# Kernel optimization log

Measured on AMD Instinct MI355X. Metric: run time of the kernel, lower is better.

Reference implementation:

```python
import jax, jax.numpy as jnp
import numpy as np

OMEGA_ENC = 0.01   # Encoder.omega
OMEGA_K = 0.1      # KernelMLP.omega
N0, E0 = 4096, 16384     # level-0 graph
N1, E1 = 1024, 8192      # level-1 (pooled) graph
F_IN, H, LAT, DIM = 8, 64, 32, 3
F = H + DIM              # conv input features (x || pos)


def _glorot(key, shape):
    s = jnp.sqrt(2.0 / (shape[0] + shape[-1]))
    return (jax.random.normal(key, shape) * s).astype(jnp.float32)


def setup_inputs() -> dict:
    key = jax.random.key(0)
    ks = jax.random.split(key, 24)
    inp = {
        "x": jax.random.normal(ks[0], (N0, F_IN), jnp.float32),
        "pos": jax.random.normal(ks[1], (N0, DIM), jnp.float32),
        "edge_index": jax.random.randint(ks[2], (2, E0), 0, N0),
        "pool_edge_index1": jax.random.randint(ks[3], (2, E1), 0, N1),
        "pool_pos1": jax.random.normal(ks[4], (N1, DIM), jnp.float32),
        "pool_keep_idx0": jnp.sort(jax.random.randint(ks[5], (N1,), 0, N0)),
        "lin0_w": _glorot(ks[6], (F_IN, H)),
        "lin0_b": 0.01 * jax.random.normal(ks[7], (H,), jnp.float32),
        "lin1_w": _glorot(ks[8], (H, LAT)),
        "lin1_b": 0.01 * jax.random.normal(ks[9], (LAT,), jnp.float32),
    }
    k = 10
    for i in range(2):
        inp[f"conv{i}_k_w0"] = _glorot(ks[k], (DIM + 1, H))
        inp[f"conv{i}_k_b0"] = 0.01 * jax.random.normal(ks[k + 1], (H,), jnp.float32)
        inp[f"conv{i}_k_w1"] = _glorot(ks[k + 2], (H, H))
        inp[f"conv{i}_k_b1"] = 0.01 * jax.random.normal(ks[k + 3], (H,), jnp.float32)
        inp[f"conv{i}_k_w2"] = _glorot(ks[k + 4], (H, F))
        inp[f"conv{i}_k_b2"] = 0.01 * jax.random.normal(ks[k + 5], (F,), jnp.float32)
        inp[f"conv{i}_bias"] = jnp.zeros((H,), jnp.float32)  # zeros() init in torch
        k += 6
    return inp


def _with_self_loops(ei, n):
    # add_remaining_self_loops: input edges are assumed self-loop-free
    loops = jnp.arange(n, dtype=ei.dtype)
    return jnp.concatenate([ei, jnp.stack([loops, loops])], axis=1)


def _kernel_conv(xf, ei, pos, n, w0, b0, w1, b1, w2, b2, bias):
    src, dst = ei[0], ei[1]
    rel = pos[dst] - pos[src]                               # [E,3]
    zero = jnp.all(rel == 0.0, axis=1)                      # self loops -> rho=0, nan phi in torch
    rel_s = jnp.where(zero[:, None], 1.0, rel)              # safe values (avoid nan grads)
    rho = jnp.sqrt(jnp.sum(rel_s * rel_s, axis=1))
    theta = jnp.arctan2(rel_s[:, 1], rel_s[:, 0])
    phi = jnp.arcsin(jnp.clip(rel_s[:, 2] / rho, -1.0, 1.0))
    # torch sets theta/phi to 0 where phi is nan (rho==0); rho itself is 0 there
    rho = jnp.where(zero, 0.0, rho)
    theta = jnp.where(zero, 0.0, theta)
    phi = jnp.where(zero, 0.0, phi)
    feats = jnp.stack([rho, theta / jnp.pi, phi / jnp.pi], axis=1)   # [E,3]
    # KernelMLP lin0 on (feats || channel_id), evaluated for all out channels at once
    base = feats @ w0[:DIM] + b0                            # [E,H]
    ch = jnp.arange(H, dtype=xf.dtype)                      # out_channels == H
    h0 = jnp.sin(OMEGA_K * (base[None] + ch[:, None, None] * w0[DIM][None, None]))  # [C,E,H]
    h1 = jnp.sin(OMEGA_K * (jnp.einsum('ceh,hk->cek', h0, w1) + b1))                # [C,E,H]
    x_j = xf[src]                                           # [E,F]
    # msg[e,c] = (lin2(h1[c,e]) * x_j[e]).sum(); lin2 folded into the contraction
    msg = jnp.einsum('ceh,hf,ef->ec', h1, w2, x_j) + (x_j @ b2)[:, None]            # [E,C]
    return jax.ops.segment_sum(msg, dst, num_segments=n) + bias


def reference(x, edge_index, pos, pool_edge_index1, pool_pos1, pool_keep_idx0,
              lin0_w, lin0_b, lin1_w, lin1_b,
              conv0_k_w0, conv0_k_b0, conv0_k_w1, conv0_k_b1, conv0_k_w2, conv0_k_b2, conv0_bias,
              conv1_k_w0, conv1_k_b0, conv1_k_w1, conv1_k_b1, conv1_k_w2, conv1_k_b2, conv1_bias):
    n0 = x.shape[0]
    h = jnp.sin(OMEGA_ENC * (x @ lin0_w + lin0_b))
    ei0 = _with_self_loops(edge_index, n0)
    h = jnp.sin(OMEGA_ENC * _kernel_conv(jnp.concatenate([h, pos], 1), ei0, pos, n0,
                                         conv0_k_w0, conv0_k_b0, conv0_k_w1, conv0_k_b1,
                                         conv0_k_w2, conv0_k_b2, conv0_bias))
    # max_pool_neighbor_x: per-node max over neighbors incl. self (self loops in ei0)
    h = jax.ops.segment_max(h[ei0[0]], ei0[1], num_segments=n0)[pool_keep_idx0]
    n1 = pool_pos1.shape[0]
    ei1 = _with_self_loops(pool_edge_index1, n1)
    h = jnp.sin(OMEGA_ENC * _kernel_conv(jnp.concatenate([h, pool_pos1], 1), ei1, pool_pos1, n1,
                                         conv1_k_w0, conv1_k_b0, conv1_k_w1, conv1_k_b1,
                                         conv1_k_w2, conv1_k_b2, conv1_bias))
    return jnp.sin(OMEGA_ENC * (h @ lin1_w + lin1_b))   # [N1, LAT]
```

## Files before the change

kernel.cpp:

```cpp
#include <hip/hip_runtime.h>
#include <hip/hip_fp16.h>

#define N0C 4096
#define E0C 16384
#define N1C 1024
#define E1C 8192
#define HC 64
#define FINC 8
#define LATC 32
#define FC 67
#define E0T (E0C + N0C)
#define E1T (E1C + N1C)

typedef float f32x4 __attribute__((ext_vector_type(4)));
typedef _Float16 f16x8 __attribute__((ext_vector_type(8)));

__global__ void k_misc(const float* __restrict__ c0w0, const float* __restrict__ c1w0,
                       const float* __restrict__ c0w1, const float* __restrict__ c1w1,
                       const float* __restrict__ c0w2, const float* __restrict__ c1w2,
                       const int* __restrict__ ei0, const int* __restrict__ ei1,
                       _Float16* __restrict__ bC0, _Float16* __restrict__ bS0,
                       _Float16* __restrict__ bC1, _Float16* __restrict__ bS1,
                       _Float16* __restrict__ w1f0, _Float16* __restrict__ w1f1,
                       float* __restrict__ w2t0, float* __restrict__ w2t1,
                       int* __restrict__ cnt) {
  int id = blockIdx.x * blockDim.x + threadIdx.x;
  if (id < 8192) {
    int lvl = id >> 12, r = id & 4095;
    int fi = r >> 9, lane = (r >> 3) & 63, j = r & 7;
    int nt = fi & 3, ks = fi >> 2;
    int c = nt * 16 + (lane & 15);
    int h = ks * 32 + (lane >> 4) * 8 + j;
    const float* w = lvl ? c1w0 : c0w0;
    float s, cv;
    sincosf(0.1f * (float)c * w[3 * HC + h], &s, &cv);
    (lvl ? bC1 : bC0)[r] = (_Float16)cv;
    (lvl ? bS1 : bS0)[r] = (_Float16)s;
  } else if (id < 16384) {
    int r0 = id - 8192;
    int lvl = r0 >> 12, r = r0 & 4095;
    int fi = r >> 9, lane = (r >> 3) & 63, j = r & 7;
    int ms = fi & 3, ks = fi >> 2;
    int h = ks * 32 + (lane >> 4) * 8 + j;
    int kout = ms * 16 + (lane & 15);
    const float* w = lvl ? c1w1 : c0w1;
    (lvl ? w1f1 : w1f0)[r] = (_Float16)w[h * HC + kout];
  } else if (id < 24960) {
    int r = id - 16384;
    int lvl = r >= FC * HC;
    r -= lvl * FC * HC;
    int f = r >> 6, k = r & 63;
    (lvl ? w2t1 : w2t0)[r] = (lvl ? c1w2 : c0w2)[k * FC + f];
  } else if (id < 54656) {
    int r = id - 24960;
    if (r < E0T) {
      int dst = (r < E0C) ? ei0[E0C + r] : (r - E0C);
      atomicAdd(cnt + dst, 1);
    } else {
      int e = r - E0T;
      int dst = (e < E1C) ? ei1[E1C + e] : (e - E1C);
      atomicAdd(cnt + N0C + dst, 1);
    }
  }
}

__global__ void k_scan(const int* __restrict__ cnt, int* __restrict__ rp0,
                       int* __restrict__ rp1) {
  __shared__ int s[1024];
  const int b = blockIdx.x;
  const int n = b ? N1C : N0C;
  const int* c = cnt + (b ? N0C : 0);
  int* rp = b ? rp1 : rp0;
  const int tid = threadIdx.x;
  const int per = n >> 10;
  int loc[4];
  int sum = 0;
  for (int j = 0; j < per; ++j) { loc[j] = c[tid * per + j]; sum += loc[j]; }
  s[tid] = sum;
  __syncthreads();
  for (int off = 1; off < 1024; off <<= 1) {
    int v = s[tid] + ((tid >= off) ? s[tid - off] : 0);
    __syncthreads();
    s[tid] = v;
    __syncthreads();
  }
  int base = tid ? s[tid - 1] : 0;
  for (int j = 0; j < per; ++j) { rp[tid * per + j] = base; base += loc[j]; }
  if (tid == 1023) rp[n] = s[1023];
}

__global__ void k_scatter(const int* __restrict__ ei0, const int* __restrict__ ei1,
                          const int* __restrict__ rp0, const int* __restrict__ rp1,
                          int* __restrict__ fill, int* __restrict__ eidx0,
                          int* __restrict__ eidx1) {
  int id = blockIdx.x * blockDim.x + threadIdx.x;
  if (id < E0T) {
    int dst = (id < E0C) ? ei0[E0C + id] : (id - E0C);
    eidx0[rp0[dst] + atomicAdd(fill + dst, 1)] = id;
  } else if (id < E0T + E1T) {
    int e = id - E0T;
    int dst = (e < E1C) ? ei1[E1C + e] : (e - E1C);
    eidx1[rp1[dst] + atomicAdd(fill + N0C + dst, 1)] = e;
  }
}

__global__ void k_node0(const float* __restrict__ x, const float* __restrict__ l0w,
                        const float* __restrict__ l0b, const float* __restrict__ posp,
                        const float* __restrict__ w2t, const float* __restrict__ b2,
                        float* __restrict__ tN, float* __restrict__ dN) {
  __shared__ float xr[4][64];
  const int wave = threadIdx.x >> 6, lane = threadIdx.x & 63;
  const int n = blockIdx.x * 4 + wave;
  float a = l0b[lane];
#pragma unroll
  for (int f = 0; f < FINC; ++f) a = fmaf(x[n * FINC + f], l0w[f * HC + lane], a);
  xr[wave][lane] = sinf(0.01f * a);
  __syncthreads();
  const float px = posp[n * 3], py = posp[n * 3 + 1], pz = posp[n * 3 + 2];
  float tl = 0.f, ds = 0.f;
#pragma unroll 8
  for (int f = 0; f < HC; ++f) {
    float xv = xr[wave][f];
    tl = fmaf(xv, w2t[f * HC + lane], tl);
    ds = fmaf(xv, b2[f], ds);
  }
  tl = fmaf(px, w2t[64 * HC + lane], fmaf(py, w2t[65 * HC + lane], fmaf(pz, w2t[66 * HC + lane], tl)));
  ds = fmaf(px, b2[64], fmaf(py, b2[65], fmaf(pz, b2[66], ds)));
  tN[n * HC + lane] = tl;
  if (lane == 0) dN[n] = ds;
}

__global__ __launch_bounds__(256, 2) void k_conv(
    const int* __restrict__ ei, int E, int eTot,
    const float* __restrict__ posp,
    const float* __restrict__ tN, const float* __restrict__ dN,
    const float* __restrict__ kw0, const float* __restrict__ kb0,
    const _Float16* __restrict__ bC, const _Float16* __restrict__ bS,
    const _Float16* __restrict__ w1f, const float* __restrict__ b1,
    float* __restrict__ msg) {
  __shared__ _Float16 scS[4][64], scC[4][64];
  const int tid = threadIdx.x;
  const int wave = tid >> 6, lane = tid & 63;
  const int q = lane >> 4;

  f16x8 w1r[8], cbr[8], sbr[8];
#pragma unroll
  for (int f = 0; f < 8; ++f) {
    w1r[f] = *(const f16x8*)(w1f + ((f << 6) + lane) * 8);
    cbr[f] = *(const f16x8*)(bC + ((f << 6) + lane) * 8);
    sbr[f] = *(const f16x8*)(bS + ((f << 6) + lane) * 8);
  }
  const float kb0v = kb0[lane];
  const float kw0x = kw0[lane], kw0y = kw0[HC + lane], kw0z = kw0[2 * HC + lane];

  const int nW = gridDim.x * 4;
  for (int e = blockIdx.x * 4 + wave; e < eTot; e += nW) {
    int s, d2;
    if (e < E) { s = ei[e]; d2 = ei[E + e]; } else { s = e - E; d2 = s; }
    const float px = posp[s * 3], py = posp[s * 3 + 1], pz = posp[s * 3 + 2];
    const float rx = posp[d2 * 3] - px;
    const float ry = posp[d2 * 3 + 1] - py;
    const float rz = posp[d2 * 3 + 2] - pz;
    float f0 = 0.f, f1 = 0.f, f2 = 0.f;
    if (!(rx == 0.f && ry == 0.f && rz == 0.f)) {
      const float PI_F = 3.14159265358979323846f;
      float rho = sqrtf(rx * rx + ry * ry + rz * rz);
      float th = atan2f(ry, rx);
      float ratio = fminf(1.f, fmaxf(-1.f, rz / rho));
      float ph = asinf(ratio);
      f0 = rho; f1 = th / PI_F; f2 = ph / PI_F;
    }
    float base = fmaf(f0, kw0x, fmaf(f1, kw0y, fmaf(f2, kw0z, kb0v)));
    float sv, cv;
    sincosf(0.1f * base, &sv, &cv);
    scS[wave][lane] = (_Float16)sv;
    scC[wave][lane] = (_Float16)cv;
    __builtin_amdgcn_wave_barrier();

    f16x8 bf[2][4];
#pragma unroll
    for (int ks = 0; ks < 2; ++ks) {
      f16x8 sv8 = *(const f16x8*)&scS[wave][ks * 32 + q * 8];
      f16x8 cv8 = *(const f16x8*)&scC[wave][ks * 32 + q * 8];
#pragma unroll
      for (int nt = 0; nt < 4; ++nt)
        bf[ks][nt] = sv8 * cbr[ks * 4 + nt] + cv8 * sbr[ks * 4 + nt];
    }

    f32x4 acc[4][4];
    const f32x4 zero = {0.f, 0.f, 0.f, 0.f};
#pragma unroll
    for (int ms = 0; ms < 4; ++ms)
#pragma unroll
      for (int nt = 0; nt < 4; ++nt) acc[ms][nt] = zero;
#pragma unroll
    for (int ks = 0; ks < 2; ++ks)
#pragma unroll
      for (int ms = 0; ms < 4; ++ms)
#pragma unroll
        for (int nt = 0; nt < 4; ++nt)
          acc[ms][nt] = __builtin_amdgcn_mfma_f32_16x16x32_f16(
              w1r[ks * 4 + ms], bf[ks][nt], acc[ms][nt], 0, 0, 0);

    const float dv = dN[s];
    float snt0 = 0.f, snt1 = 0.f, snt2 = 0.f, snt3 = 0.f;
#pragma unroll
    for (int ms = 0; ms < 4; ++ms) {
      f32x4 tv = *(const f32x4*)(tN + (size_t)s * HC + ms * 16 + q * 4);
      f32x4 bv = *(const f32x4*)(b1 + ms * 16 + q * 4);
#pragma unroll
      for (int r = 0; r < 4; ++r) {
        float bb = 0.1f * bv[r], tt = tv[r];
        snt0 = fmaf(__sinf(fmaf(0.1f, acc[ms][0][r], bb)), tt, snt0);
        snt1 = fmaf(__sinf(fmaf(0.1f, acc[ms][1][r], bb)), tt, snt1);
        snt2 = fmaf(__sinf(fmaf(0.1f, acc[ms][2][r], bb)), tt, snt2);
        snt3 = fmaf(__sinf(fmaf(0.1f, acc[ms][3][r], bb)), tt, snt3);
      }
    }
    snt0 += __shfl_xor(snt0, 16, 64); snt0 += __shfl_xor(snt0, 32, 64);
    snt1 += __shfl_xor(snt1, 16, 64); snt1 += __shfl_xor(snt1, 32, 64);
    snt2 += __shfl_xor(snt2, 16, 64); snt2 += __shfl_xor(snt2, 32, 64);
    snt3 += __shfl_xor(snt3, 16, 64); snt3 += __shfl_xor(snt3, 32, 64);
    float val = (q == 0) ? snt0 : (q == 1) ? snt1 : (q == 2) ? snt2 : snt3;
    msg[(size_t)e * HC + lane] = val + dv;
  }
}

__global__ void k_reduce(const float* __restrict__ msg, const int* __restrict__ eidx,
                         const int* __restrict__ rp, const float* __restrict__ bias,
                         float* __restrict__ outp, int n) {
  int wave = threadIdx.x >> 6, lane = threadIdx.x & 63;
  int node = blockIdx.x * 4 + wave;
  if (node >= n) return;
  int j0 = rp[node], j1 = rp[node + 1];
  float s = 0.f;
  for (int j = j0; j < j1; ++j) s += msg[(size_t)eidx[j] * HC + lane];
  outp[node * HC + lane] = sinf(0.01f * (s + bias[lane]));
}

__global__ void k_pool1(const float* __restrict__ hc0, const int* __restrict__ eidx,
                        const int* __restrict__ rp, const int* __restrict__ ei,
                        const int* __restrict__ keep, const float* __restrict__ ppos,
                        const float* __restrict__ w2t, const float* __restrict__ b2,
                        float* __restrict__ tN, float* __restrict__ dN) {
  __shared__ float xr[4][64];
  const int wave = threadIdx.x >> 6, lane = threadIdx.x & 63;
  const int i = blockIdx.x * 4 + wave;
  int n = keep[i];
  int j0 = rp[n], j1 = rp[n + 1];
  float m = -INFINITY;
  for (int j = j0; j < j1; ++j) {
    int e = eidx[j];
    int src = (e < E0C) ? ei[e] : (e - E0C);
    m = fmaxf(m, hc0[(size_t)src * HC + lane]);
  }
  xr[wave][lane] = m;
  __syncthreads();
  const float px = ppos[i * 3], py = ppos[i * 3 + 1], pz = ppos[i * 3 + 2];
  float tl = 0.f, ds = 0.f;
#pragma unroll 8
  for (int f = 0; f < HC; ++f) {
    float xv = xr[wave][f];
    tl = fmaf(xv, w2t[f * HC + lane], tl);
    ds = fmaf(xv, b2[f], ds);
  }
  tl = fmaf(px, w2t[64 * HC + lane], fmaf(py, w2t[65 * HC + lane], fmaf(pz, w2t[66 * HC + lane], tl)));
  ds = fmaf(px, b2[64], fmaf(py, b2[65], fmaf(pz, b2[66], ds)));
  tN[i * HC + lane] = tl;
  if (lane == 0) dN[i] = ds;
}

__global__ void k_reduce1f(const float* __restrict__ msg, const int* __restrict__ eidx,
                           const int* __restrict__ rp, const float* __restrict__ bias,
                           const float* __restrict__ l1w, const float* __restrict__ l1b,
                           float* __restrict__ outp) {
  __shared__ float hr[4][64];
  const int wave = threadIdx.x >> 6, lane = threadIdx.x & 63;
  const int node = blockIdx.x * 4 + wave;
  int j0 = rp[node], j1 = rp[node + 1];
  float s = 0.f;
  for (int j = j0; j < j1; ++j) s += msg[(size_t)eidx[j] * HC + lane];
  hr[wave][lane] = sinf(0.01f * (s + bias[lane]));
  __syncthreads();
  if (lane < 32) {
    float o = l1b[lane];
#pragma unroll 8
    for (int c = 0; c < HC; ++c) o = fmaf(hr[wave][c], l1w[c * LATC + lane], o);
    outp[node * LATC + lane] = sinf(0.01f * o);
  }
}

extern "C" void kernel_launch(void* const* d_in, const int* in_sizes, int n_in,
                              void* d_out, int out_size, void* d_ws, size_t ws_size,
                              hipStream_t stream) {
  (void)in_sizes; (void)n_in; (void)out_size; (void)ws_size;
  const float* x    = (const float*)d_in[0];
  const float* pos  = (const float*)d_in[1];
  const int*   ei   = (const int*)d_in[2];
  const int*   pei  = (const int*)d_in[3];
  const float* ppos = (const float*)d_in[4];
  const int*   keep = (const int*)d_in[5];
  const float* l0w  = (const float*)d_in[6];
  const float* l0b  = (const float*)d_in[7];
  const float* l1w  = (const float*)d_in[8];
  const float* l1b  = (const float*)d_in[9];
  const float* c0w0 = (const float*)d_in[10];
  const float* c0b0 = (const float*)d_in[11];
  const float* c0w1 = (const float*)d_in[12];
  const float* c0b1 = (const float*)d_in[13];
  const float* c0w2 = (const float*)d_in[14];
  const float* c0b2 = (const float*)d_in[15];
  const float* c0bias = (const float*)d_in[16];
  const float* c1w0 = (const float*)d_in[17];
  const float* c1b0 = (const float*)d_in[18];
  const float* c1w1 = (const float*)d_in[19];
  const float* c1b1 = (const float*)d_in[20];
  const float* c1w2 = (const float*)d_in[21];
  const float* c1b2 = (const float*)d_in[22];
  const float* c1bias = (const float*)d_in[23];
  float* outp = (float*)d_out;

  char* p = (char*)d_ws;
  auto carve = [&](size_t bytes) -> char* {
    char* r = p;
    p += (bytes + 255) & ~(size_t)255;
    return r;
  };
  float* hc0  = (float*)carve((size_t)N0C * HC * 4);
  float* tN0  = (float*)carve((size_t)N0C * HC * 4);
  float* dN0  = (float*)carve((size_t)N0C * 4);
  float* tN1  = (float*)carve((size_t)N1C * HC * 4);
  float* dN1  = (float*)carve((size_t)N1C * 4);
  _Float16* bC0  = (_Float16*)carve(4096 * 2);
  _Float16* bS0  = (_Float16*)carve(4096 * 2);
  _Float16* bC1  = (_Float16*)carve(4096 * 2);
  _Float16* bS1  = (_Float16*)carve(4096 * 2);
  _Float16* w1f0 = (_Float16*)carve(4096 * 2);
  _Float16* w1f1 = (_Float16*)carve(4096 * 2);
  float* w2t0 = (float*)carve((size_t)FC * HC * 4);
  float* w2t1 = (float*)carve((size_t)FC * HC * 4);
  int* cnt  = (int*)carve((size_t)(N0C + N1C) * 4);
  int* fill = (int*)carve((size_t)(N0C + N1C) * 4);
  int* rp0 = (int*)carve((size_t)(N0C + 1) * 4);
  int* rp1 = (int*)carve((size_t)(N1C + 1) * 4);
  int* eidx0 = (int*)carve((size_t)E0T * 4);
  int* eidx1 = (int*)carve((size_t)E1T * 4);
  float* msg = (float*)carve((size_t)E0T * HC * 4);

  hipMemsetAsync(cnt, 0, (size_t)(N0C + N1C) * 4 * 2, stream);

  k_misc<<<214, 256, 0, stream>>>(c0w0, c1w0, c0w1, c1w1, c0w2, c1w2, ei, pei,
                                  bC0, bS0, bC1, bS1, w1f0, w1f1, w2t0, w2t1, cnt);
  k_scan<<<2, 1024, 0, stream>>>(cnt, rp0, rp1);
  k_scatter<<<(E0T + E1T + 255) / 256, 256, 0, stream>>>(ei, pei, rp0, rp1, fill,
                                                         eidx0, eidx1);
  k_node0<<<N0C / 4, 256, 0, stream>>>(x, l0w, l0b, pos, w2t0, c0b2, tN0, dN0);

  k_conv<<<512, 256, 0, stream>>>(ei, E0C, E0T, pos, tN0, dN0, c0w0, c0b0,
                                  bC0, bS0, w1f0, c0b1, msg);
  k_reduce<<<N0C / 4, 256, 0, stream>>>(msg, eidx0, rp0, c0bias, hc0, N0C);
  k_pool1<<<N1C / 4, 256, 0, stream>>>(hc0, eidx0, rp0, ei, keep, ppos, w2t1, c1b2,
                                       tN1, dN1);

  k_conv<<<512, 256, 0, stream>>>(pei, E1C, E1T, ppos, tN1, dN1, c1w0, c1b0,
                                  bC1, bS1, w1f1, c1b1, msg);
  k_reduce1f<<<N1C / 4, 256, 0, stream>>>(msg, eidx1, rp1, c1bias, l1w, l1b, outp);
}
```

Measured before the change: 194.4 us.

## Fuse node prep into setup kernel and software-pipeline the edge conv kernel

Merges the node-0 projection into the weight-prep/count kernel and drops the separate w2 transpose by staging w2 into shared memory in the node kernels. The conv kernel now handles a fixed four edges per wave, prefetching the next edge's geometry and dN while the current MFMA runs. It also moves the cos/sin basis tables to LDS, folds the 0.1 scale into w1 and the bias into the accumulator init, and raises occupancy to 3 blocks. Scan becomes a wave-shuffle scan and the reduce loops are unrolled by two. These changes target launch overhead, register pressure and per-edge latency, at the cost of more LDS traffic and one large grid per conv.

```diff
diff --git a/kernel.cpp b/kernel.cpp
--- a/kernel.cpp
+++ b/kernel.cpp
@@ -15,78 +15,114 @@
 typedef float f32x4 __attribute__((ext_vector_type(4)));
 typedef _Float16 f16x8 __attribute__((ext_vector_type(8)));
 
-__global__ void k_misc(const float* __restrict__ c0w0, const float* __restrict__ c1w0,
-                       const float* __restrict__ c0w1, const float* __restrict__ c1w1,
-                       const float* __restrict__ c0w2, const float* __restrict__ c1w2,
-                       const int* __restrict__ ei0, const int* __restrict__ ei1,
-                       _Float16* __restrict__ bC0, _Float16* __restrict__ bS0,
-                       _Float16* __restrict__ bC1, _Float16* __restrict__ bS1,
-                       _Float16* __restrict__ w1f0, _Float16* __restrict__ w1f1,
-                       float* __restrict__ w2t0, float* __restrict__ w2t1,
-                       int* __restrict__ cnt) {
-  int id = blockIdx.x * blockDim.x + threadIdx.x;
-  if (id < 8192) {
-    int lvl = id >> 12, r = id & 4095;
-    int fi = r >> 9, lane = (r >> 3) & 63, j = r & 7;
-    int nt = fi & 3, ks = fi >> 2;
-    int c = nt * 16 + (lane & 15);
-    int h = ks * 32 + (lane >> 4) * 8 + j;
-    const float* w = lvl ? c1w0 : c0w0;
-    float s, cv;
-    sincosf(0.1f * (float)c * w[3 * HC + h], &s, &cv);
-    (lvl ? bC1 : bC0)[r] = (_Float16)cv;
-    (lvl ? bS1 : bS0)[r] = (_Float16)s;
-  } else if (id < 16384) {
-    int r0 = id - 8192;
-    int lvl = r0 >> 12, r = r0 & 4095;
-    int fi = r >> 9, lane = (r >> 3) & 63, j = r & 7;
-    int ms = fi & 3, ks = fi >> 2;
-    int h = ks * 32 + (lane >> 4) * 8 + j;
-    int kout = ms * 16 + (lane & 15);
-    const float* w = lvl ? c1w1 : c0w1;
-    (lvl ? w1f1 : w1f0)[r] = (_Float16)w[h * HC + kout];
-  } else if (id < 24960) {
-    int r = id - 16384;
-    int lvl = r >= FC * HC;
-    r -= lvl * FC * HC;
-    int f = r >> 6, k = r & 63;
-    (lvl ? w2t1 : w2t0)[r] = (lvl ? c1w2 : c0w2)[k * FC + f];
-  } else if (id < 54656) {
-    int r = id - 24960;
-    if (r < E0T) {
-      int dst = (r < E0C) ? ei0[E0C + r] : (r - E0C);
-      atomicAdd(cnt + dst, 1);
-    } else {
-      int e = r - E0T;
-      int dst = (e < E1C) ? ei1[E1C + e] : (e - E1C);
-      atomicAdd(cnt + N0C + dst, 1);
+__global__ __launch_bounds__(256) void k_prep(
+    const float* __restrict__ x, const float* __restrict__ l0w,
+    const float* __restrict__ l0b, const float* __restrict__ posp,
+    const float* __restrict__ c0w2, const float* __restrict__ c0b2,
+    const float* __restrict__ c0w0, const float* __restrict__ c1w0,
+    const float* __restrict__ c0w1, const float* __restrict__ c1w1,
+    const int* __restrict__ ei0, const int* __restrict__ ei1,
+    _Float16* __restrict__ bC0, _Float16* __restrict__ bS0,
+    _Float16* __restrict__ bC1, _Float16* __restrict__ bS1,
+    _Float16* __restrict__ w1f0, _Float16* __restrict__ w1f1,
+    int* __restrict__ cnt, float* __restrict__ tN, float* __restrict__ dN) {
+  if (blockIdx.x < 1024) {
+    __shared__ float w2s[64][69];
+    __shared__ float xr[4][64];
+    const int tid = threadIdx.x;
+    const int wave = __builtin_amdgcn_readfirstlane(tid >> 6), lane = tid & 63;
+    for (int idx = tid; idx < HC * FC; idx += 256)
+      w2s[idx / FC][idx % FC] = c0w2[idx];
+    const int n = blockIdx.x * 4 + wave;
+    float a = l0b[lane];
+#pragma unroll
+    for (int f = 0; f < FINC; ++f) a = fmaf(x[n * FINC + f], l0w[f * HC + lane], a);
+    xr[wave][lane] = sinf(0.01f * a);
+    __syncthreads();
+    const float px = posp[n * 3], py = posp[n * 3 + 1], pz = posp[n * 3 + 2];
+    float tl = 0.f, ds = 0.f;
+#pragma unroll 8
+    for (int f = 0; f < HC; ++f) {
+      float xv = xr[wave][f];
+      tl = fmaf(xv, w2s[lane][f], tl);
+      ds = fmaf(xv, c0b2[f], ds);
+    }
+    tl = fmaf(px, w2s[lane][64], fmaf(py, w2s[lane][65], fmaf(pz, w2s[lane][66], tl)));
+    ds = fmaf(px, c0b2[64], fmaf(py, c0b2[65], fmaf(pz, c0b2[66], ds)));
+    tN[n * HC + lane] = tl;
+    if (lane == 0) dN[n] = ds;
+  } else {
+    int id = (blockIdx.x - 1024) * 256 + threadIdx.x;
+    if (id < 8192) {
+      int lvl = id >> 12, r = id & 4095;
+      int fi = r >> 9, lane = (r >> 3) & 63, j = r & 7;
+      int nt = fi & 3, ks = fi >> 2;
+      int c = nt * 16 + (lane & 15);
+      int h = ks * 32 + (lane >> 4) * 8 + j;
+      const float* w = lvl ? c1w0 : c0w0;
+      float s, cv;
+      sincosf(0.1f * (float)c * w[3 * HC + h], &s, &cv);
+      (lvl ? bC1 : bC0)[r] = (_Float16)cv;
+      (lvl ? bS1 : bS0)[r] = (_Float16)s;
+    } else if (id < 16384) {
+      int r0 = id - 8192;
+      int lvl = r0 >> 12, r = r0 & 4095;
+      int fi = r >> 9, lane = (r >> 3) & 63, j = r & 7;
+      int ms = fi & 3, ks = fi >> 2;
+      int h = ks * 32 + (lane >> 4) * 8 + j;
+      int kout = ms * 16 + (lane & 15);
+      const float* w = lvl ? c1w1 : c0w1;
+      (lvl ? w1f1 : w1f0)[r] = (_Float16)(0.1f * w[h * HC + kout]);
+    } else if (id < 16384 + E0T + E1T) {
+      int r = id - 16384;
+      if (r < E0T) {
+        int dst = (r < E0C) ? ei0[E0C + r] : (r - E0C);
+        atomicAdd(cnt + dst, 1);
+      } else {
+        int e = r - E0T;
+        int dst = (e < E1C) ? ei1[E1C + e] : (e - E1C);
+        atomicAdd(cnt + N0C + dst, 1);
+      }
     }
   }
 }
 
 __global__ void k_scan(const int* __restrict__ cnt, int* __restrict__ rp0,
                        int* __restrict__ rp1) {
-  __shared__ int s[1024];
+  __shared__ int wsum[16];
   const int b = blockIdx.x;
   const int n = b ? N1C : N0C;
   const int* c = cnt + (b ? N0C : 0);
   int* rp = b ? rp1 : rp0;
   const int tid = threadIdx.x;
+  const int lane = tid & 63, wid = tid >> 6;
   const int per = n >> 10;
   int loc[4];
   int sum = 0;
   for (int j = 0; j < per; ++j) { loc[j] = c[tid * per + j]; sum += loc[j]; }
-  s[tid] = sum;
+  int xv = sum;
+#pragma unroll
+  for (int off = 1; off < 64; off <<= 1) {
+    int v = __shfl_up(xv, off, 64);
+    if (lane >= off) xv += v;
+  }
+  if (lane == 63) wsum[wid] = xv;
   __syncthreads();
-  for (int off = 1; off < 1024; off <<= 1) {
-    int v = s[tid] + ((tid >= off) ? s[tid - off] : 0);
-    __syncthreads();
-    s[tid] = v;
-    __syncthreads();
-  }
-  int base = tid ? s[tid - 1] : 0;
+  if (wid == 0) {
+    int w = (lane < 16) ? wsum[lane] : 0;
+#pragma unroll
+    for (int off = 1; off < 16; off <<= 1) {
+      int v = __shfl_up(w, off, 64);
+      if (lane >= off) w += v;
+    }
+    if (lane < 16) wsum[lane] = w;
+  }
+  __syncthreads();
+  int prefix = wid ? wsum[wid - 1] : 0;
+  int incl = xv + prefix;
+  int base = incl - sum;
   for (int j = 0; j < per; ++j) { rp[tid * per + j] = base; base += loc[j]; }
-  if (tid == 1023) rp[n] = s[1023];
+  if (tid == 1023) rp[n] = incl;
 }
 
 __global__ void k_scatter(const int* __restrict__ ei0, const int* __restrict__ ei1,
@@ -104,59 +140,42 @@
   }
 }
 
-__global__ void k_node0(const float* __restrict__ x, const float* __restrict__ l0w,
-                        const float* __restrict__ l0b, const float* __restrict__ posp,
-                        const float* __restrict__ w2t, const float* __restrict__ b2,
-                        float* __restrict__ tN, float* __restrict__ dN) {
-  __shared__ float xr[4][64];
-  const int wave = threadIdx.x >> 6, lane = threadIdx.x & 63;
-  const int n = blockIdx.x * 4 + wave;
-  float a = l0b[lane];
-#pragma unroll
-  for (int f = 0; f < FINC; ++f) a = fmaf(x[n * FINC + f], l0w[f * HC + lane], a);
-  xr[wave][lane] = sinf(0.01f * a);
-  __syncthreads();
-  const float px = posp[n * 3], py = posp[n * 3 + 1], pz = posp[n * 3 + 2];
-  float tl = 0.f, ds = 0.f;
-#pragma unroll 8
-  for (int f = 0; f < HC; ++f) {
-    float xv = xr[wave][f];
-    tl = fmaf(xv, w2t[f * HC + lane], tl);
-    ds = fmaf(xv, b2[f], ds);
-  }
-  tl = fmaf(px, w2t[64 * HC + lane], fmaf(py, w2t[65 * HC + lane], fmaf(pz, w2t[66 * HC + lane], tl)));
-  ds = fmaf(px, b2[64], fmaf(py, b2[65], fmaf(pz, b2[66], ds)));
-  tN[n * HC + lane] = tl;
-  if (lane == 0) dN[n] = ds;
-}
-
-__global__ __launch_bounds__(256, 2) void k_conv(
-    const int* __restrict__ ei, int E, int eTot,
+__global__ __launch_bounds__(256, 3) void k_conv(
+    const int* __restrict__ ei, int E,
     const float* __restrict__ posp,
     const float* __restrict__ tN, const float* __restrict__ dN,
     const float* __restrict__ kw0, const float* __restrict__ kb0,
     const _Float16* __restrict__ bC, const _Float16* __restrict__ bS,
     const _Float16* __restrict__ w1f, const float* __restrict__ b1,
     float* __restrict__ msg) {
-  __shared__ _Float16 scS[4][64], scC[4][64];
+  __shared__ __attribute__((aligned(16))) _Float16 bCs[4096], bSs[4096];
+  __shared__ __attribute__((aligned(16))) _Float16 scS[4][2][64], scC[4][2][64];
   const int tid = threadIdx.x;
-  const int wave = tid >> 6, lane = tid & 63;
+  const int wave = __builtin_amdgcn_readfirstlane(tid >> 6), lane = tid & 63;
   const int q = lane >> 4;
-
-  f16x8 w1r[8], cbr[8], sbr[8];
-#pragma unroll
-  for (int f = 0; f < 8; ++f) {
-    w1r[f] = *(const f16x8*)(w1f + ((f << 6) + lane) * 8);
-    cbr[f] = *(const f16x8*)(bC + ((f << 6) + lane) * 8);
-    sbr[f] = *(const f16x8*)(bS + ((f << 6) + lane) * 8);
+  for (int idx = tid; idx < 512; idx += 256) {
+    ((f16x8*)bCs)[idx] = ((const f16x8*)bC)[idx];
+    ((f16x8*)bSs)[idx] = ((const f16x8*)bS)[idx];
+  }
+  f16x8 w1r[8];
+#pragma unroll
+  for (int f = 0; f < 8; ++f) w1r[f] = *(const f16x8*)(w1f + ((f << 6) + lane) * 8);
+  f32x4 bbq[4];
+#pragma unroll
+  for (int ms = 0; ms < 4; ++ms) {
+    f32x4 t = *(const f32x4*)(b1 + ms * 16 + q * 4);
+    bbq[ms] = t * 0.1f;
   }
   const float kb0v = kb0[lane];
   const float kw0x = kw0[lane], kw0y = kw0[HC + lane], kw0z = kw0[2 * HC + lane];
-
-  const int nW = gridDim.x * 4;
-  for (int e = blockIdx.x * 4 + wave; e < eTot; e += nW) {
+  __syncthreads();
+
+  const int e0 = (blockIdx.x * 4 + wave) * 4;
+
+  auto stg = [&](int e, int& sN, float& sv, float& cv, float& dv) {
     int s, d2;
     if (e < E) { s = ei[e]; d2 = ei[E + e]; } else { s = e - E; d2 = s; }
+    sN = s;
     const float px = posp[s * 3], py = posp[s * 3 + 1], pz = posp[s * 3 + 2];
     const float rx = posp[d2 * 3] - px;
     const float ry = posp[d2 * 3 + 1] - py;
@@ -171,50 +190,63 @@
       f0 = rho; f1 = th / PI_F; f2 = ph / PI_F;
     }
     float base = fmaf(f0, kw0x, fmaf(f1, kw0y, fmaf(f2, kw0z, kb0v)));
-    float sv, cv;
     sincosf(0.1f * base, &sv, &cv);
-    scS[wave][lane] = (_Float16)sv;
-    scC[wave][lane] = (_Float16)cv;
+    dv = dN[s];
+  };
+
+  int s0;
+  float sv0, cv0, dv0;
+  stg(e0, s0, sv0, cv0, dv0);
+#pragma unroll
+  for (int i = 0; i < 4; ++i) {
+    const int buf = i & 1;
+    scS[wave][buf][lane] = (_Float16)sv0;
+    scC[wave][buf][lane] = (_Float16)cv0;
     __builtin_amdgcn_wave_barrier();
-
-    f16x8 bf[2][4];
+    f32x4 tr[4];
+    {
+      const float* trp = tN + (size_t)s0 * HC;
+#pragma unroll
+      for (int ms = 0; ms < 4; ++ms) tr[ms] = *(const f32x4*)(trp + ms * 16 + q * 4);
+    }
+    int s1 = 0;
+    float sv1 = 0.f, cv1 = 0.f, dv1 = 0.f;
+    if (i < 3) stg(e0 + i + 1, s1, sv1, cv1, dv1);
+
+    f32x4 acc[4][4];
+#pragma unroll
+    for (int ms = 0; ms < 4; ++ms)
+#pragma unroll
+      for (int nt = 0; nt < 4; ++nt) acc[ms][nt] = bbq[ms];
 #pragma unroll
     for (int ks = 0; ks < 2; ++ks) {
-      f16x8 sv8 = *(const f16x8*)&scS[wave][ks * 32 + q * 8];
-      f16x8 cv8 = *(const f16x8*)&scC[wave][ks * 32 + q * 8];
-#pragma unroll
-      for (int nt = 0; nt < 4; ++nt)
-        bf[ks][nt] = sv8 * cbr[ks * 4 + nt] + cv8 * sbr[ks * 4 + nt];
-    }
-
-    f32x4 acc[4][4];
-    const f32x4 zero = {0.f, 0.f, 0.f, 0.f};
-#pragma unroll
-    for (int ms = 0; ms < 4; ++ms)
-#pragma unroll
-      for (int nt = 0; nt < 4; ++nt) acc[ms][nt] = zero;
-#pragma unroll
-    for (int ks = 0; ks < 2; ++ks)
+      f16x8 sv8 = *(const f16x8*)&scS[wave][buf][ks * 32 + q * 8];
+      f16x8 cv8 = *(const f16x8*)&scC[wave][buf][ks * 32 + q * 8];
+      f16x8 bf[4];
+#pragma unroll
+      for (int nt = 0; nt < 4; ++nt) {
+        f16x8 cb = *(const f16x8*)&bCs[((ks * 4 + nt) * 64 + lane) * 8];
+        f16x8 sb = *(const f16x8*)&bSs[((ks * 4 + nt) * 64 + lane) * 8];
+        bf[nt] = sv8 * cb + cv8 * sb;
+      }
 #pragma unroll
       for (int ms = 0; ms < 4; ++ms)
 #pragma unroll
         for (int nt = 0; nt < 4; ++nt)
           acc[ms][nt] = __builtin_amdgcn_mfma_f32_16x16x32_f16(
-              w1r[ks * 4 + ms], bf[ks][nt], acc[ms][nt], 0, 0, 0);
-
-    const float dv = dN[s];
+              w1r[ks * 4 + ms], bf[nt], acc[ms][nt], 0, 0, 0);
+    }
+
     float snt0 = 0.f, snt1 = 0.f, snt2 = 0.f, snt3 = 0.f;
 #pragma unroll
     for (int ms = 0; ms < 4; ++ms) {
-      f32x4 tv = *(const f32x4*)(tN + (size_t)s * HC + ms * 16 + q * 4);
-      f32x4 bv = *(const f32x4*)(b1 + ms * 16 + q * 4);
 #pragma unroll
       for (int r = 0; r < 4; ++r) {
-        float bb = 0.1f * bv[r], tt = tv[r];
-        snt0 = fmaf(__sinf(fmaf(0.1f, acc[ms][0][r], bb)), tt, snt0);
-        snt1 = fmaf(__sinf(fmaf(0.1f, acc[ms][1][r], bb)), tt, snt1);
-        snt2 = fmaf(__sinf(fmaf(0.1f, acc[ms][2][r], bb)), tt, snt2);
-        snt3 = fmaf(__sinf(fmaf(0.1f, acc[ms][3][r], bb)), tt, snt3);
+        float tt = tr[ms][r];
+        snt0 = fmaf(__sinf(acc[ms][0][r]), tt, snt0);
+        snt1 = fmaf(__sinf(acc[ms][1][r]), tt, snt1);
+        snt2 = fmaf(__sinf(acc[ms][2][r]), tt, snt2);
+        snt3 = fmaf(__sinf(acc[ms][3][r]), tt, snt3);
       }
     }
     snt0 += __shfl_xor(snt0, 16, 64); snt0 += __shfl_xor(snt0, 32, 64);
@@ -222,29 +254,39 @@
     snt2 += __shfl_xor(snt2, 16, 64); snt2 += __shfl_xor(snt2, 32, 64);
     snt3 += __shfl_xor(snt3, 16, 64); snt3 += __shfl_xor(snt3, 32, 64);
     float val = (q == 0) ? snt0 : (q == 1) ? snt1 : (q == 2) ? snt2 : snt3;
-    msg[(size_t)e * HC + lane] = val + dv;
-  }
-}
-
-__global__ void k_reduce(const float* __restrict__ msg, const int* __restrict__ eidx,
-                         const int* __restrict__ rp, const float* __restrict__ bias,
-                         float* __restrict__ outp, int n) {
-  int wave = threadIdx.x >> 6, lane = threadIdx.x & 63;
-  int node = blockIdx.x * 4 + wave;
-  if (node >= n) return;
-  int j0 = rp[node], j1 = rp[node + 1];
-  float s = 0.f;
-  for (int j = j0; j < j1; ++j) s += msg[(size_t)eidx[j] * HC + lane];
-  outp[node * HC + lane] = sinf(0.01f * (s + bias[lane]));
+    msg[(size_t)(e0 + i) * HC + lane] = val + dv0;
+    s0 = s1; sv0 = sv1; cv0 = cv1; dv0 = dv1;
+  }
+}
+
+__global__ void k_reduce0(const float* __restrict__ msg, const int* __restrict__ eidx,
+                          const int* __restrict__ rp, const float* __restrict__ bias,
+                          float* __restrict__ hc) {
+  const int wave = threadIdx.x >> 6, lane = threadIdx.x & 63;
+  const int n = blockIdx.x * 4 + wave;
+  const int j0 = rp[n], j1 = rp[n + 1];
+  float a0 = 0.f, a1 = 0.f;
+  int j = j0;
+  for (; j + 1 < j1; j += 2) {
+    int ea = eidx[j], eb = eidx[j + 1];
+    a0 += msg[(size_t)ea * HC + lane];
+    a1 += msg[(size_t)eb * HC + lane];
+  }
+  if (j < j1) a0 += msg[(size_t)eidx[j] * HC + lane];
+  hc[(size_t)n * HC + lane] = sinf(0.01f * (a0 + a1 + bias[lane]));
 }
 
 __global__ void k_pool1(const float* __restrict__ hc0, const int* __restrict__ eidx,
                         const int* __restrict__ rp, const int* __restrict__ ei,
                         const int* __restrict__ keep, const float* __restrict__ ppos,
-                        const float* __restrict__ w2t, const float* __restrict__ b2,
+                        const float* __restrict__ c1w2, const float* __restrict__ c1b2,
                         float* __restrict__ tN, float* __restrict__ dN) {
+  __shared__ float w2s[64][69];
   __shared__ float xr[4][64];
-  const int wave = threadIdx.x >> 6, lane = threadIdx.x & 63;
+  const int tid = threadIdx.x;
+  const int wave = __builtin_amdgcn_readfirstlane(tid >> 6), lane = tid & 63;
+  for (int idx = tid; idx < HC * FC; idx += 256)
+    w2s[idx / FC][idx % FC] = c1w2[idx];
   const int i = blockIdx.x * 4 + wave;
   int n = keep[i];
   int j0 = rp[n], j1 = rp[n + 1];
@@ -261,11 +303,11 @@
 #pragma unroll 8
   for (int f = 0; f < HC; ++f) {
     float xv = xr[wave][f];
-    tl = fmaf(xv, w2t[f * HC + lane], tl);
-    ds = fmaf(xv, b2[f], ds);
-  }
-  tl = fmaf(px, w2t[64 * HC + lane], fmaf(py, w2t[65 * HC + lane], fmaf(pz, w2t[66 * HC + lane], tl)));
-  ds = fmaf(px, b2[64], fmaf(py, b2[65], fmaf(pz, b2[66], ds)));
+    tl = fmaf(xv, w2s[lane][f], tl);
+    ds = fmaf(xv, c1b2[f], ds);
+  }
+  tl = fmaf(px, w2s[lane][64], fmaf(py, w2s[lane][65], fmaf(pz, w2s[lane][66], tl)));
+  ds = fmaf(px, c1b2[64], fmaf(py, c1b2[65], fmaf(pz, c1b2[66], ds)));
   tN[i * HC + lane] = tl;
   if (lane == 0) dN[i] = ds;
 }
@@ -277,15 +319,22 @@
   __shared__ float hr[4][64];
   const int wave = threadIdx.x >> 6, lane = threadIdx.x & 63;
   const int node = blockIdx.x * 4 + wave;
-  int j0 = rp[node], j1 = rp[node + 1];
-  float s = 0.f;
-  for (int j = j0; j < j1; ++j) s += msg[(size_t)eidx[j] * HC + lane];
-  hr[wave][lane] = sinf(0.01f * (s + bias[lane]));
+  const int j0 = rp[node], j1 = rp[node + 1];
+  float a0 = 0.f, a1 = 0.f;
+  int j = j0;
+  for (; j + 1 < j1; j += 2) {
+    int ea = eidx[j], eb = eidx[j + 1];
+    a0 += msg[(size_t)ea * HC + lane];
+    a1 += msg[(size_t)eb * HC + lane];
+  }
+  if (j < j1) a0 += msg[(size_t)eidx[j] * HC + lane];
+  hr[wave][lane] = sinf(0.01f * (a0 + a1 + bias[lane]));
   __syncthreads();
-  if (lane < 32) {
+  if (lane < LATC) {
+    const float* h = hr[wave];
     float o = l1b[lane];
 #pragma unroll 8
-    for (int c = 0; c < HC; ++c) o = fmaf(hr[wave][c], l1w[c * LATC + lane], o);
+    for (int c = 0; c < HC; ++c) o = fmaf(h[c], l1w[c * LATC + lane], o);
     outp[node * LATC + lane] = sinf(0.01f * o);
   }
 }
@@ -337,8 +386,6 @@
   _Float16* bS1  = (_Float16*)carve(4096 * 2);
   _Float16* w1f0 = (_Float16*)carve(4096 * 2);
   _Float16* w1f1 = (_Float16*)carve(4096 * 2);
-  float* w2t0 = (float*)carve((size_t)FC * HC * 4);
-  float* w2t1 = (float*)carve((size_t)FC * HC * 4);
   int* cnt  = (int*)carve((size_t)(N0C + N1C) * 4);
   int* fill = (int*)carve((size_t)(N0C + N1C) * 4);
   int* rp0 = (int*)carve((size_t)(N0C + 1) * 4);
@@ -349,20 +396,19 @@
 
   hipMemsetAsync(cnt, 0, (size_t)(N0C + N1C) * 4 * 2, stream);
 
-  k_misc<<<214, 256, 0, stream>>>(c0w0, c1w0, c0w1, c1w1, c0w2, c1w2, ei, pei,
-                                  bC0, bS0, bC1, bS1, w1f0, w1f1, w2t0, w2t1, cnt);
+  k_prep<<<1024 + 180, 256, 0, stream>>>(x, l0w, l0b, pos, c0w2, c0b2,
+                                         c0w0, c1w0, c0w1, c1w1, ei, pei,
+                                         bC0, bS0, bC1, bS1, w1f0, w1f1,
+                                         cnt, tN0, dN0);
   k_scan<<<2, 1024, 0, stream>>>(cnt, rp0, rp1);
   k_scatter<<<(E0T + E1T + 255) / 256, 256, 0, stream>>>(ei, pei, rp0, rp1, fill,
                                                          eidx0, eidx1);
-  k_node0<<<N0C / 4, 256, 0, stream>>>(x, l0w, l0b, pos, w2t0, c0b2, tN0, dN0);
-
-  k_conv<<<512, 256, 0, stream>>>(ei, E0C, E0T, pos, tN0, dN0, c0w0, c0b0,
-                                  bC0, bS0, w1f0, c0b1, msg);
-  k_reduce<<<N0C / 4, 256, 0, stream>>>(msg, eidx0, rp0, c0bias, hc0, N0C);
-  k_pool1<<<N1C / 4, 256, 0, stream>>>(hc0, eidx0, rp0, ei, keep, ppos, w2t1, c1b2,
-                                       tN1, dN1);
-
-  k_conv<<<512, 256, 0, stream>>>(pei, E1C, E1T, ppos, tN1, dN1, c1w0, c1b0,
-                                  bC1, bS1, w1f1, c1b1, msg);
+  k_conv<<<E0T / 16, 256, 0, stream>>>(ei, E0C, pos, tN0, dN0, c0w0, c0b0,
+                                       bC0, bS0, w1f0, c0b1, msg);
+  k_reduce0<<<N0C / 4, 256, 0, stream>>>(msg, eidx0, rp0, c0bias, hc0);
+  k_pool1<<<N1C / 4, 256, 0, stream>>>(hc0, eidx0, rp0, ei, keep, ppos,
+                                       c1w2, c1b2, tN1, dN1);
+  k_conv<<<E1T / 16, 256, 0, stream>>>(pei, E1C, ppos, tN1, dN1, c1w0, c1b0,
+                                       bC1, bS1, w1f1, c1b1, msg);
   k_reduce1f<<<N1C / 4, 256, 0, stream>>>(msg, eidx1, rp1, c1bias, l1w, l1b, outp);
 }
```

Measured after the change: 193.6 us. No clear change (-0.5%).
